# Optimization experiments

Measured on AMD Instinct MI355X. Metric: run time of the kernel, lower is better.

The kernel has to match this reference:

```python
import jax, jax.numpy as jnp
import numpy as np

CURV = 0.9            # geoopt PoincareBall(0.9)
SQRT_C = CURV ** 0.5
MIN_NORM = 1e-15
PROJ_EPS = 4e-3       # geoopt float32 boundary eps
ATANH_EPS = 1e-7
COS_EPS = 1e-8        # torch.cosine_similarity eps


def _norm(x):
    return jnp.sqrt(jnp.maximum(jnp.sum(x * x, axis=-1, keepdims=True), MIN_NORM * MIN_NORM))


def _project(x):
    # project onto ball of radius (1-eps)/sqrt(c)
    n = jnp.maximum(_norm(x), MIN_NORM)
    maxnorm = (1.0 - PROJ_EPS) / SQRT_C
    return jnp.where(n > maxnorm, x / n * maxnorm, x)


def expmap0(u):
    n = jnp.maximum(_norm(u), MIN_NORM)
    gamma = jnp.tanh(SQRT_C * n) * u / (SQRT_C * n)
    return _project(gamma)


def mobius_add(x, y):
    c = CURV
    x2 = jnp.sum(x * x, axis=-1, keepdims=True)
    y2 = jnp.sum(y * y, axis=-1, keepdims=True)
    xy = jnp.sum(x * y, axis=-1, keepdims=True)
    num = (1.0 + 2.0 * c * xy + c * y2) * x + (1.0 - c * x2) * y
    den = 1.0 + 2.0 * c * xy + c * c * x2 * y2
    return num / jnp.maximum(den, MIN_NORM)


def pdist(x, y):
    # dist(x,y) = 2/sqrt(c) * artanh(sqrt(c) * ||(-x) (+) y||)
    d = mobius_add(-x, y)
    n = _norm(d)[..., 0]
    z = jnp.clip(SQRT_C * n, -1.0 + ATANH_EPS, 1.0 - ATANH_EPS)
    return 2.0 / SQRT_C * jnp.arctanh(z)


def cos_sim(a, b):
    na = jnp.maximum(jnp.sqrt(jnp.sum(a * a, axis=-1)), COS_EPS)
    nb = jnp.maximum(jnp.sqrt(jnp.sum(b * b, axis=-1)), COS_EPS)
    return jnp.sum(a * b, axis=-1) / (na * nb)


def setup_inputs() -> dict:
    key = jax.random.key(0)
    ks = jax.random.split(key, 11)
    B, L, Ls, C, Lc, H, R = 4, 512, 128, 20, 128, 768, 512
    s = 0.02  # keep projected embeddings in a realistic range
    return {
        "text_out": jax.random.normal(ks[0], (B, L, H), jnp.float32),
        "summary_out": jax.random.normal(ks[1], (B, Ls, H), jnp.float32),
        "candidate_out": jax.random.normal(ks[2], (B, C, Lc, H), jnp.float32),
        "W_d": jax.random.normal(ks[3], (H, R), jnp.float32) * s,
        "W_s": jax.random.normal(ks[4], (H, R), jnp.float32) * s,
        "W_c": jax.random.normal(ks[5], (H, R), jnp.float32) * s,
        "W_p": jax.random.normal(ks[6], (R, R), jnp.float32) * s,
        "conv_w1": jax.random.normal(ks[7], (1, H, R), jnp.float32) * s,
        "conv_b1": jax.random.normal(ks[8], (R,), jnp.float32) * s,
        "conv_w2": jax.random.normal(ks[9], (2, H, R), jnp.float32) * s,
        "conv_b2": jax.random.normal(ks[10], (R,), jnp.float32) * s,
    }


def _forward(text_out, summary_out, candidate_out, W_d, W_s, W_c, W_p,
             conv_w1, conv_b1, conv_w2, conv_b2):
    # --- document ---
    doc_emb = expmap0(text_out[:, 0, :] @ W_d)                       # [B,R]

    # NGramers (max_gram=2, eval mode so dropout is identity)
    x = text_out[:, 1:-1, :]                                         # [B,L-2,H]
    y1 = jax.nn.relu(jnp.einsum('blh,hr->blr', x, conv_w1[0]) + conv_b1)
    y2 = jax.nn.relu(jnp.einsum('blh,hr->blr', x[:, :-1], conv_w2[0])
                     + jnp.einsum('blh,hr->blr', x[:, 1:], conv_w2[1]) + conv_b2)
    gram = jnp.concatenate([y1, y2], axis=1)                         # [B,2L-5,R]

    doc_word_emb = expmap0(jnp.einsum('blr,rk->blk', gram, W_p))     # [B,T,R]
    doc_inter = 1.0 / pdist(doc_word_emb, doc_emb[:, None, :])       # [B,T]

    # --- summary ---
    summary_emb = expmap0(jnp.max(summary_out, axis=1) @ W_s)        # [B,R]
    summary_score = -pdist(summary_emb, doc_emb) ** 2                # [B]
    sum_inter = 1.0 / pdist(doc_word_emb, summary_emb[:, None, :])   # [B,T]
    summary_score = summary_score + cos_sim(doc_inter, sum_inter)    # [B]

    # --- candidates ---
    cand_emb = expmap0(jnp.einsum('bch,hr->bcr', jnp.max(candidate_out, axis=2), W_c))  # [B,C,R]
    score = -pdist(cand_emb, doc_emb[:, None, :]) ** 2               # [B,C]
    cand_inter = 1.0 / pdist(doc_word_emb[:, None, :, :], cand_emb[:, :, None, :])      # [B,C,T]
    score = score + cos_sim(doc_inter[:, None, :], cand_inter)       # [B,C]
    return score, summary_score


def reference(text_out, summary_out, candidate_out, W_d, W_s, W_c, W_p,
              conv_w1, conv_b1, conv_w2, conv_b2):
    return _forward(text_out, summary_out, candidate_out, W_d, W_s, W_c, W_p,
                    conv_w1, conv_b1, conv_w2, conv_b2)
```

## Files before the change

kernel.cpp:

```cpp
#include <hip/hip_runtime.h>
#include <math.h>

#define SQRTC  0.94868329805051381f
#define MAXN   (0.996f/SQRTC)
#define OME_CLIP (1.0f - 0.996f*0.996f)
#define TWO_OVER_SQRTC 2.1081851067789197f

typedef unsigned short u16;
typedef __attribute__((ext_vector_type(8))) short bf8;
typedef __attribute__((ext_vector_type(4))) float f4;

__device__ __forceinline__ u16 f2bf(float f){
    union { float f; unsigned int i; } v; v.f = f;
    unsigned int x = v.i;
    unsigned int lsb = (x >> 16) & 1u;
    x += 0x7fffu + lsb;
    return (u16)(x >> 16);
}
__device__ __forceinline__ float bf2f(u16 u){
    union { unsigned int i; float f; } v; v.i = ((unsigned int)u) << 16; return v.f;
}

__device__ __forceinline__ void gload16(void* lds, const void* g){
    __builtin_amdgcn_global_load_lds(
        (const __attribute__((address_space(1))) unsigned int*)g,
        (__attribute__((address_space(3))) unsigned int*)lds,
        16, 0, 0);
}

__device__ __forceinline__ float pdist_stable(float ome_x, float ome_y, float t){
    float u = 1.0f - ome_x, v = 1.0f - ome_y;
    float den = fmaxf(1.0f - 1.8f*t + u*v, 1e-15f);
    float q = ome_x*ome_y/den;
    q = fminf(fmaxf(q, 2.0e-7f), 1.0f);
    float z = sqrtf(fmaxf(1.0f - q, 0.0f));
    float at = 0.5f * logf((1.0f+z)*(1.0f+z)/q);
    return TWO_OVER_SQRTC * at;
}

__device__ __forceinline__ void expmap_scale_ome(float sum, float* fout, float* omeout){
    float nraw = sqrtf(fmaxf(sum, 1e-30f));
    float n = fmaxf(nraw, 1e-15f);
    float sn = SQRTC*n;
    float th = tanhf(sn);
    float factor = th/sn;
    float gn = factor*nraw;
    if (gn > MAXN){ *fout = factor*(MAXN/gn); *omeout = OME_CLIP; }
    else { *fout = factor; *omeout = fmaxf((1.0f-th)*(1.0f+th), 1e-12f); }
}

__global__ __launch_bounds__(256)
void k_stage1(const float* __restrict__ summ, const float* __restrict__ cand,
              const float* __restrict__ text,
              const float* __restrict__ w1, const float* __restrict__ w2,
              const float* __restrict__ wp,
              float* __restrict__ smax, float* __restrict__ cmax,
              u16* __restrict__ textb, u16* __restrict__ w1t,
              u16* __restrict__ w2t, u16* __restrict__ wpt)
{
    __shared__ float shm[1056];
    int bx = blockIdx.x;
    int t = threadIdx.x;
    if (bx < 252){
        int row = bx / 3, hc = bx - row*3;
        int w = t >> 6, lane = t & 63;
        const float* in = (row < 4) ? (summ + (long long)row*128*768)
                                    : (cand + (long long)(row-4)*128*768);
        const float* p = in + (long long)(w*32)*768 + hc*256 + lane*4;
        float4 m = make_float4(-INFINITY,-INFINITY,-INFINITY,-INFINITY);
        #pragma unroll 8
        for (int l = 0; l < 32; l++){
            float4 v = *(const float4*)(p + (long long)l*768);
            m.x = fmaxf(m.x, v.x); m.y = fmaxf(m.y, v.y);
            m.z = fmaxf(m.z, v.z); m.w = fmaxf(m.w, v.w);
        }
        float4* sm4 = (float4*)shm;
        sm4[w*64 + lane] = m; __syncthreads();
        if (t < 64){
            float4 a = sm4[t], b4 = sm4[64+t], c4 = sm4[128+t], d4 = sm4[192+t];
            float4 r;
            r.x = fmaxf(fmaxf(a.x,b4.x), fmaxf(c4.x,d4.x));
            r.y = fmaxf(fmaxf(a.y,b4.y), fmaxf(c4.y,d4.y));
            r.z = fmaxf(fmaxf(a.z,b4.z), fmaxf(c4.z,d4.z));
            r.w = fmaxf(fmaxf(a.w,b4.w), fmaxf(c4.w,d4.w));
            float* outp = (row < 4) ? (smax + row*768) : (cmax + (row-4)*768);
            *(float4*)(outp + hc*256 + t*4) = r;
        }
        return;
    }
    int pb = bx - 252;
    if (pb < 768){
        int base = pb*2048 + t*8;
        float4 a = *(const float4*)(text + base);
        float4 b = *(const float4*)(text + base + 4);
        *(ushort4*)(textb + base)     = make_ushort4(f2bf(a.x), f2bf(a.y), f2bf(a.z), f2bf(a.w));
        *(ushort4*)(textb + base + 4) = make_ushort4(f2bf(b.x), f2bf(b.y), f2bf(b.z), f2bf(b.w));
        return;
    }
    int j = pb - 768;
    const float* in; u16* outp; int K;
    if (j < 384){ in = w1; outp = w1t; K = 768; }
    else if (j < 1152){ j -= 384; in = w2; outp = w2t; K = 1536; }
    else { j -= 1152; in = wp; outp = wpt; K = 512; }
    const int N = 512, ntile = N/32;
    int k0 = (j/ntile)*32, n0 = (j - (j/ntile)*ntile)*32;
    int tx = t & 31, ty = t >> 5;
    #pragma unroll
    for (int i = 0; i < 4; i++)
        shm[(ty*4+i)*33 + tx] = in[(long long)(k0 + ty*4 + i)*N + n0 + tx];
    __syncthreads();
    #pragma unroll
    for (int i = 0; i < 4; i++)
        outp[(long long)(n0 + ty*4 + i)*K + k0 + tx] = f2bf(shm[tx*33 + ty*4+i]);
}

__global__ __launch_bounds__(256)
void k_stage2(const u16* __restrict__ textb,
              const u16* __restrict__ w1t, const u16* __restrict__ w2t,
              const float* __restrict__ cb1, const float* __restrict__ cb2,
              const float* __restrict__ text,
              const float* __restrict__ smax, const float* __restrict__ cmax,
              const float* __restrict__ W_d, const float* __restrict__ W_s,
              const float* __restrict__ W_c,
              u16* __restrict__ gram, float* __restrict__ emb_all)
{
    __shared__ char smem[32768];
    int bx = blockIdx.x;
    int t = threadIdx.x;
    if (bx < 512){
        u16* As0 = (u16*)smem;
        u16* Bs0 = (u16*)(smem + 8192);
        u16* As1 = (u16*)(smem + 16384);
        u16* Bs1 = (u16*)(smem + 24576);
        int xx = bx & 63, yy = bx >> 6;
        int job = xx & 1;
        int m0 = (xx >> 1) * 64;
        int n0 = yy * 64;
        int K   = job ? 1536 : 768;
        int M   = job ? 2036 : 2040;
        int rpb = job ? 509 : 510;
        int ob  = job ? 510 : 0;
        const u16* Bt = job ? w2t : w1t;
        const float* bias = job ? cb2 : cb1;

        int r0 = t >> 3;
        int co = (((t & 7) ^ (r0 & 7)) << 3);

        int gm0 = m0 + r0;      if (gm0 >= M) gm0 = M - 1;
        int gm1 = m0 + r0 + 32; if (gm1 >= M) gm1 = M - 1;
        int ab0 = gm0 / rpb, al0 = gm0 - ab0*rpb;
        int ab1 = gm1 / rpb, al1 = gm1 - ab1*rpb;
        const u16* a0 = textb + (long long)ab0*393216 + (long long)(al0+1)*768 + co;
        const u16* a1 = textb + (long long)ab1*393216 + (long long)(al1+1)*768 + co;
        const u16* bp0 = Bt + (long long)(n0 + r0)*K      + co;
        const u16* bp1 = Bt + (long long)(n0 + r0 + 32)*K + co;
        int d0 = t*8, d1 = (256 + t)*8;

        int lane = t & 63, wv = t >> 6;
        int fm = lane & 15, fq = lane >> 4;
        int arow = wv*16 + fm;
        int aswz = arow & 7, bswz = fm & 7;
        int aoff0 = arow*64 + ((fq     ^ aswz) << 3);
        int aoff1 = arow*64 + (((4+fq) ^ aswz) << 3);
        int boff0 = ((fq     ^ bswz) << 3);
        int boff1 = (((4+fq) ^ bswz) << 3);

        f4 acc0 = {0,0,0,0}, acc1 = {0,0,0,0}, acc2 = {0,0,0,0}, acc3 = {0,0,0,0};
        const int nt = K >> 6;
        gload16(As0 + d0, a0);
        gload16(As0 + d1, a1);
        gload16(Bs0 + d0, bp0);
        gload16(Bs0 + d1, bp1);
        for (int i = 0; i < nt; i++){
            u16* Ac = (i & 1) ? As1 : As0;
            u16* Bc = (i & 1) ? Bs1 : Bs0;
            if (i + 1 < nt){
                u16* An = (i & 1) ? As0 : As1;
                u16* Bn = (i & 1) ? Bs0 : Bs1;
                int kn = (i + 1) << 6;
                gload16(An + d0, a0 + kn);
                gload16(An + d1, a1 + kn);
                gload16(Bn + d0, bp0 + kn);
                gload16(Bn + d1, bp1 + kn);
                asm volatile("s_waitcnt vmcnt(4)" ::: "memory");
            } else {
                asm volatile("s_waitcnt vmcnt(0)" ::: "memory");
            }
            __builtin_amdgcn_s_barrier();
            bf8 af0 = *(const bf8*)(Ac + aoff0);
            bf8 af1 = *(const bf8*)(Ac + aoff1);
            bf8 b00 = *(const bf8*)(Bc + (fm   )*64 + boff0);
            bf8 b10 = *(const bf8*)(Bc + (16+fm)*64 + boff0);
            bf8 b20 = *(const bf8*)(Bc + (32+fm)*64 + boff0);
            bf8 b30 = *(const bf8*)(Bc + (48+fm)*64 + boff0);
            bf8 b01 = *(const bf8*)(Bc + (fm   )*64 + boff1);
            bf8 b11 = *(const bf8*)(Bc + (16+fm)*64 + boff1);
            bf8 b21 = *(const bf8*)(Bc + (32+fm)*64 + boff1);
            bf8 b31 = *(const bf8*)(Bc + (48+fm)*64 + boff1);
            acc0 = __builtin_amdgcn_mfma_f32_16x16x32_bf16(af0, b00, acc0, 0, 0, 0);
            acc1 = __builtin_amdgcn_mfma_f32_16x16x32_bf16(af0, b10, acc1, 0, 0, 0);
            acc2 = __builtin_amdgcn_mfma_f32_16x16x32_bf16(af0, b20, acc2, 0, 0, 0);
            acc3 = __builtin_amdgcn_mfma_f32_16x16x32_bf16(af0, b30, acc3, 0, 0, 0);
            acc0 = __builtin_amdgcn_mfma_f32_16x16x32_bf16(af1, b01, acc0, 0, 0, 0);
            acc1 = __builtin_amdgcn_mfma_f32_16x16x32_bf16(af1, b11, acc1, 0, 0, 0);
            acc2 = __builtin_amdgcn_mfma_f32_16x16x32_bf16(af1, b21, acc2, 0, 0, 0);
            acc3 = __builtin_amdgcn_mfma_f32_16x16x32_bf16(af1, b31, acc3, 0, 0, 0);
            __builtin_amdgcn_s_barrier();
        }
        int col = n0 + fm;
        float bv0 = bias[col], bv1 = bias[col+16], bv2 = bias[col+32], bv3 = bias[col+48];
        #pragma unroll
        for (int i = 0; i < 4; i++){
            int row = m0 + wv*16 + fq*4 + i;
            if (row >= M) continue;
            int b = row/rpb, l = row - b*rpb;
            long long orow = (long long)b*1019 + ob + l;
            u16* gp = gram + orow*512;
            gp[col]      = f2bf(fmaxf(acc0[i] + bv0, 0.f));
            gp[col + 16] = f2bf(fmaxf(acc1[i] + bv1, 0.f));
            gp[col + 32] = f2bf(fmaxf(acc2[i] + bv2, 0.f));
            gp[col + 48] = f2bf(fmaxf(acc3[i] + bv3, 0.f));
        }
        return;
    }
    {
        int eb = bx - 512;
        int row = eb >> 3, nt = eb & 7;
        float* a   = (float*)smem;
        float* red = (float*)smem + 768;
        const float* A; const float* W;
        if (row < 4){ A = text + (long long)row*512*768; W = W_d; }
        else if (row < 8){ A = smax + (long long)(row-4)*768; W = W_s; }
        else { A = cmax + (long long)(row-8)*768; W = W_c; }
        for (int k = t; k < 768; k += 256) a[k] = A[k];
        __syncthreads();
        int lane = t & 63, kg = t >> 6;
        int col = nt*64 + lane;
        const float* Wp = W + (long long)(kg*192)*512 + col;
        float acc = 0.f;
        #pragma unroll 8
        for (int k = 0; k < 192; k++) acc += a[kg*192 + k] * Wp[k*512];
        red[t] = acc; __syncthreads();
        if (t < 64) emb_all[(long long)row*512 + col] = red[t] + red[t+64] + red[t+128] + red[t+192];
    }
}

__global__ __launch_bounds__(256)
void k_stage3(const u16* __restrict__ gram, const u16* __restrict__ wpt,
              u16* __restrict__ dwe_b,
              float* __restrict__ emb_all, float* __restrict__ ome_all,
              u16* __restrict__ emb_b)
{
    __shared__ char smem[32768];
    int bx = blockIdx.x;
    int t = threadIdx.x;
    if (bx < 512){
        u16* As0 = (u16*)smem;
        u16* Bs0 = (u16*)(smem + 8192);
        u16* As1 = (u16*)(smem + 16384);
        u16* Bs1 = (u16*)(smem + 24576);
        const int K = 512, M = 4076;
        int m0 = (bx >> 3) * 64;
        int n0 = (bx & 7) * 64;

        int r0 = t >> 3;
        int co = (((t & 7) ^ (r0 & 7)) << 3);
        int gm0 = m0 + r0;      if (gm0 >= M) gm0 = M - 1;
        int gm1 = m0 + r0 + 32; if (gm1 >= M) gm1 = M - 1;
        const u16* a0 = gram + (long long)gm0*512 + co;
        const u16* a1 = gram + (long long)gm1*512 + co;
        const u16* bp0 = wpt + (long long)(n0 + r0)*K      + co;
        const u16* bp1 = wpt + (long long)(n0 + r0 + 32)*K + co;
        int d0 = t*8, d1 = (256 + t)*8;

        int lane = t & 63, wv = t >> 6;
        int fm = lane & 15, fq = lane >> 4;
        int arow = wv*16 + fm;
        int aswz = arow & 7, bswz = fm & 7;
        int aoff0 = arow*64 + ((fq     ^ aswz) << 3);
        int aoff1 = arow*64 + (((4+fq) ^ aswz) << 3);
        int boff0 = ((fq     ^ bswz) << 3);
        int boff1 = (((4+fq) ^ bswz) << 3);

        f4 acc0 = {0,0,0,0}, acc1 = {0,0,0,0}, acc2 = {0,0,0,0}, acc3 = {0,0,0,0};
        const int nt = K >> 6;
        gload16(As0 + d0, a0);
        gload16(As0 + d1, a1);
        gload16(Bs0 + d0, bp0);
        gload16(Bs0 + d1, bp1);
        for (int i = 0; i < nt; i++){
            u16* Ac = (i & 1) ? As1 : As0;
            u16* Bc = (i & 1) ? Bs1 : Bs0;
            if (i + 1 < nt){
                u16* An = (i & 1) ? As0 : As1;
                u16* Bn = (i & 1) ? Bs0 : Bs1;
                int kn = (i + 1) << 6;
                gload16(An + d0, a0 + kn);
                gload16(An + d1, a1 + kn);
                gload16(Bn + d0, bp0 + kn);
                gload16(Bn + d1, bp1 + kn);
                asm volatile("s_waitcnt vmcnt(4)" ::: "memory");
            } else {
                asm volatile("s_waitcnt vmcnt(0)" ::: "memory");
            }
            __builtin_amdgcn_s_barrier();
            bf8 af0 = *(const bf8*)(Ac + aoff0);
            bf8 af1 = *(const bf8*)(Ac + aoff1);
            bf8 b00 = *(const bf8*)(Bc + (fm   )*64 + boff0);
            bf8 b10 = *(const bf8*)(Bc + (16+fm)*64 + boff0);
            bf8 b20 = *(const bf8*)(Bc + (32+fm)*64 + boff0);
            bf8 b30 = *(const bf8*)(Bc + (48+fm)*64 + boff0);
            bf8 b01 = *(const bf8*)(Bc + (fm   )*64 + boff1);
            bf8 b11 = *(const bf8*)(Bc + (16+fm)*64 + boff1);
            bf8 b21 = *(const bf8*)(Bc + (32+fm)*64 + boff1);
            bf8 b31 = *(const bf8*)(Bc + (48+fm)*64 + boff1);
            acc0 = __builtin_amdgcn_mfma_f32_16x16x32_bf16(af0, b00, acc0, 0, 0, 0);
            acc1 = __builtin_amdgcn_mfma_f32_16x16x32_bf16(af0, b10, acc1, 0, 0, 0);
            acc2 = __builtin_amdgcn_mfma_f32_16x16x32_bf16(af0, b20, acc2, 0, 0, 0);
            acc3 = __builtin_amdgcn_mfma_f32_16x16x32_bf16(af0, b30, acc3, 0, 0, 0);
            acc0 = __builtin_amdgcn_mfma_f32_16x16x32_bf16(af1, b01, acc0, 0, 0, 0);
            acc1 = __builtin_amdgcn_mfma_f32_16x16x32_bf16(af1, b11, acc1, 0, 0, 0);
            acc2 = __builtin_amdgcn_mfma_f32_16x16x32_bf16(af1, b21, acc2, 0, 0, 0);
            acc3 = __builtin_amdgcn_mfma_f32_16x16x32_bf16(af1, b31, acc3, 0, 0, 0);
            __builtin_amdgcn_s_barrier();
        }
        int col = n0 + fm;
        #pragma unroll
        for (int i = 0; i < 4; i++){
            int row = m0 + wv*16 + fq*4 + i;
            if (row >= M) continue;
            u16* dp = dwe_b + (long long)row*512;
            dp[col]      = f2bf(acc0[i]);
            dp[col + 16] = f2bf(acc1[i]);
            dp[col + 32] = f2bf(acc2[i]);
            dp[col + 48] = f2bf(acc3[i]);
        }
        return;
    }
    {
        float* red = (float*)smem;
        int row = bx - 512;
        float* X = emb_all + (long long)row*512;
        float2 u = *(float2*)(X + t*2);
        red[t] = u.x*u.x + u.y*u.y; __syncthreads();
        for (int s = 128; s > 0; s >>= 1){ if (t < s) red[t] += red[t+s]; __syncthreads(); }
        float f, ome;
        expmap_scale_ome(red[0], &f, &ome);
        float sx = u.x*f, sy = u.y*f;
        *(float2*)(X + t*2) = make_float2(sx, sy);
        u16* Xb = emb_b + (long long)row*512;
        Xb[t*2]   = f2bf(sx);
        Xb[t*2+1] = f2bf(sy);
        if (t == 0) ome_all[row] = ome;
    }
}

__global__ __launch_bounds__(64)
void k_dots_mfma(const u16* __restrict__ dwe_b, const u16* __restrict__ emb_b,
                 const float* __restrict__ ome_all,
                 float* __restrict__ doc_inter, float* __restrict__ sum_inter,
                 float* __restrict__ cand_inter)
{
    int bx = blockIdx.x;
    int b  = bx >> 6;
    int m0 = (bx & 63) * 16;
    int t = threadIdx.x;
    int fm = t & 15, fq = t >> 4;

    int arow = m0 + fm; if (arow > 1018) arow = 1018;
    const u16* Ap = dwe_b + ((long long)(b*1019 + arow))*512 + fq*8;

    int n1 = 16 + fm; if (n1 > 21) n1 = 21;
    int e0 = (fm == 0) ? b : (fm == 1) ? 4 + b : 8 + b*20 + (fm - 2);
    int e1 = 8 + b*20 + (n1 - 2);
    const u16* B0 = emb_b + (long long)e0*512 + fq*8;
    const u16* B1 = emb_b + (long long)e1*512 + fq*8;
    float oy0 = ome_all[e0];
    float oy1 = ome_all[e1];

    f4 acc0 = {0,0,0,0}, acc1 = {0,0,0,0};
    float ssq = 0.f;
    #pragma unroll 4
    for (int k0 = 0; k0 < 512; k0 += 32){
        bf8 av  = *(const bf8*)(Ap + k0);
        bf8 bv0 = *(const bf8*)(B0 + k0);
        bf8 bv1 = *(const bf8*)(B1 + k0);
        #pragma unroll
        for (int j = 0; j < 8; j++){ float x = bf2f(((u16*)&av)[j]); ssq += x*x; }
        acc0 = __builtin_amdgcn_mfma_f32_16x16x32_bf16(av, bv0, acc0, 0, 0, 0);
        acc1 = __builtin_amdgcn_mfma_f32_16x16x32_bf16(av, bv1, acc1, 0, 0, 0);
    }
    ssq += __shfl_xor(ssq, 16);
    ssq += __shfl_xor(ssq, 32);

    #pragma unroll
    for (int i = 0; i < 4; i++){
        int r = fq*4 + i;
        float rs = __shfl(ssq, r);
        int row = m0 + r;
        if (row >= 1019) continue;
        float f, ox;
        expmap_scale_ome(rs, &f, &ox);
        long long grow = (long long)b*1019 + row;
        {
            float s = acc0[i] * f;
            float dist = pdist_stable(ox, oy0, s);
            float inv = 1.0f/fmaxf(dist, 1e-12f);
            if (fm == 0) doc_inter[grow] = inv;
            else if (fm == 1) sum_inter[grow] = inv;
            else cand_inter[((long long)(b*20 + (fm - 2)))*1019 + row] = inv;
        }
        if (16 + fm < 22){
            float s = acc1[i] * f;
            float dist = pdist_stable(ox, oy1, s);
            float inv = 1.0f/fmaxf(dist, 1e-12f);
            cand_inter[((long long)(b*20 + (16 + fm - 2)))*1019 + row] = inv;
        }
    }
}

__global__ __launch_bounds__(256)
void k_final(const float* __restrict__ doc_inter, const float* __restrict__ sum_inter,
             const float* __restrict__ cand_inter,
             const float* __restrict__ emb_all, const float* __restrict__ ome_all,
             float* __restrict__ out)
{
    __shared__ float r0[256], r1[256], r2[256], r3[256];
    int j = blockIdx.x, t = threadIdx.x;
    int b; const float *a, *bb; int xi, yi; int outIdx;
    if (j < 80){
        b = j/20;
        a  = doc_inter + b*1019;
        bb = cand_inter + (long long)j*1019;
        xi = 8 + j; yi = b;
        outIdx = j;
    } else {
        b = j - 80;
        a  = doc_inter + b*1019;
        bb = sum_inter + b*1019;
        xi = 4 + b; yi = b;
        outIdx = 80 + b;
    }
    const float* xe = emb_all + (long long)xi*512;
    const float* ye = emb_all + (long long)yi*512;
    float ox = ome_all[xi], oy = ome_all[yi];
    float saa = 0.f, sbb = 0.f, sab = 0.f, st = 0.f;
    for (int l = t; l < 1019; l += 256){ float av = a[l], bv = bb[l]; saa += av*av; sbb += bv*bv; sab += av*bv; }
    for (int k = t; k < 512; k += 256) st += xe[k]*ye[k];
    r0[t] = saa; r1[t] = sbb; r2[t] = sab; r3[t] = st; __syncthreads();
    for (int s = 128; s > 0; s >>= 1){
        if (t < s){ r0[t] += r0[t+s]; r1[t] += r1[t+s]; r2[t] += r2[t+s]; r3[t] += r3[t+s]; }
        __syncthreads();
    }
    if (t == 0){
        float na = fmaxf(sqrtf(r0[0]), 1e-8f);
        float nb = fmaxf(sqrtf(r1[0]), 1e-8f);
        float cosv = r2[0] / (na*nb);
        float pd = pdist_stable(ox, oy, r3[0]);
        out[outIdx] = -pd*pd + cosv;
    }
}

extern "C" void kernel_launch(void* const* d_in, const int* in_sizes, int n_in,
                              void* d_out, int out_size, void* d_ws, size_t ws_size,
                              hipStream_t stream) {
    const float* text = (const float*)d_in[0];
    const float* summ = (const float*)d_in[1];
    const float* cand = (const float*)d_in[2];
    const float* W_d  = (const float*)d_in[3];
    const float* W_s  = (const float*)d_in[4];
    const float* W_c  = (const float*)d_in[5];
    const float* W_p  = (const float*)d_in[6];
    const float* cw1  = (const float*)d_in[7];
    const float* cb1  = (const float*)d_in[8];
    const float* cw2  = (const float*)d_in[9];
    const float* cb2  = (const float*)d_in[10];
    float* out = (float*)d_out;

    const int B = 4, C = 20, H = 768;

    char* base = (char*)d_ws;
    size_t off = 0;
    auto allocF = [&](size_t n)->float*{ float* p = (float*)(base + off); off += ((n*4) + 255) & ~(size_t)255; return p; };
    auto allocU = [&](size_t n)->u16*{ u16* p = (u16*)(base + off); off += ((n*2) + 255) & ~(size_t)255; return p; };

    float* smax = allocF(B*H);
    float* cmax = allocF(B*C*H);
    float* emb_all = allocF(88*512);
    float* ome_all = allocF(88);
    u16* emb_b = allocU(88*512);
    u16* textb = allocU(4*512*768);
    u16* w1t   = allocU(512*768);
    u16* w2t   = allocU(512*1536);
    u16* wpt   = allocU(512*512);
    u16* gram  = allocU(4076*512);
    u16* dwe_b = allocU(4076*512);
    float* doc_inter = allocF(4076);
    float* sum_inter = allocF(4076);
    float* cand_inter= allocF(B*C*1019);

    k_stage1<<<2428, 256, 0, stream>>>(summ, cand, text, cw1, cw2, W_p,
                                       smax, cmax, textb, w1t, w2t, wpt);

    k_stage2<<<1216, 256, 0, stream>>>(textb, w1t, w2t, cb1, cb2,
                                       text, smax, cmax, W_d, W_s, W_c,
                                       gram, emb_all);

    k_stage3<<<600, 256, 0, stream>>>(gram, wpt, dwe_b, emb_all, ome_all, emb_b);

    k_dots_mfma<<<256, 64, 0, stream>>>(dwe_b, emb_b, ome_all,
                                        doc_inter, sum_inter, cand_inter);

    k_final<<<84, 256, 0, stream>>>(doc_inter, sum_inter, cand_inter,
                                    emb_all, ome_all, out);
}
```

Baseline: 139.9 us.

## Fuse final cosine/pdist reduction into MFMA dots kernel via atomics and last-block finish

Removes the k_final launch and the doc/sum/cand_inter intermediate buffers. Each dots block now reduces its per-row inverse distances into squared-norm and dot-product partial sums and adds them to a small global accumulator with atomics. A ticket counter lets the last block compute the cosine similarities and final scores, and block 0 also computes the embedding dot products. This saves one kernel launch and the global round trip, at the cost of atomic contention, a serial 84-iteration loop in block 0, and float atomics whose order is not deterministic.

```diff
diff --git a/kernel.cpp b/kernel.cpp
--- a/kernel.cpp
+++ b/kernel.cpp
@@ -49,6 +49,14 @@
     else { *fout = factor; *omeout = fmaxf((1.0f-th)*(1.0f+th), 1e-12f); }
 }
 
+#define ACC_SDD 0
+#define ACC_SSS 4
+#define ACC_SDS 8
+#define ACC_SCC 12
+#define ACC_SDC 92
+#define ACC_CTR 172
+#define ACC_PD  176
+
 __global__ __launch_bounds__(256)
 void k_stage1(const float* __restrict__ summ, const float* __restrict__ cand,
               const float* __restrict__ text,
@@ -56,11 +64,13 @@
               const float* __restrict__ wp,
               float* __restrict__ smax, float* __restrict__ cmax,
               u16* __restrict__ textb, u16* __restrict__ w1t,
-              u16* __restrict__ w2t, u16* __restrict__ wpt)
+              u16* __restrict__ w2t, u16* __restrict__ wpt,
+              float* __restrict__ accum)
 {
     __shared__ float shm[1056];
     int bx = blockIdx.x;
     int t = threadIdx.x;
+    if (bx == 0 && t < 176) accum[t] = 0.0f;
     if (bx < 252){
         int row = bx / 3, hc = bx - row*3;
         int w = t >> 6, lane = t & 63;
@@ -357,9 +367,8 @@
 
 __global__ __launch_bounds__(64)
 void k_dots_mfma(const u16* __restrict__ dwe_b, const u16* __restrict__ emb_b,
-                 const float* __restrict__ ome_all,
-                 float* __restrict__ doc_inter, float* __restrict__ sum_inter,
-                 float* __restrict__ cand_inter)
+                 const float* __restrict__ ome_all, const float* __restrict__ emb_all,
+                 float* __restrict__ accum, float* __restrict__ out)
 {
     int bx = blockIdx.x;
     int b  = bx >> 6;
@@ -393,71 +402,89 @@
     ssq += __shfl_xor(ssq, 16);
     ssq += __shfl_xor(ssq, 32);
 
+    float cc0 = 0.f, dc0 = 0.f, cc1 = 0.f, dc1 = 0.f;
     #pragma unroll
     for (int i = 0; i < 4; i++){
         int r = fq*4 + i;
         float rs = __shfl(ssq, r);
         int row = m0 + r;
-        if (row >= 1019) continue;
         float f, ox;
         expmap_scale_ome(rs, &f, &ox);
-        long long grow = (long long)b*1019 + row;
+        float inv0, inv1;
         {
             float s = acc0[i] * f;
             float dist = pdist_stable(ox, oy0, s);
-            float inv = 1.0f/fmaxf(dist, 1e-12f);
-            if (fm == 0) doc_inter[grow] = inv;
-            else if (fm == 1) sum_inter[grow] = inv;
-            else cand_inter[((long long)(b*20 + (fm - 2)))*1019 + row] = inv;
-        }
-        if (16 + fm < 22){
+            inv0 = 1.0f/fmaxf(dist, 1e-12f);
+        }
+        {
             float s = acc1[i] * f;
             float dist = pdist_stable(ox, oy1, s);
-            float inv = 1.0f/fmaxf(dist, 1e-12f);
-            cand_inter[((long long)(b*20 + (16 + fm - 2)))*1019 + row] = inv;
-        }
-    }
-}
-
-__global__ __launch_bounds__(256)
-void k_final(const float* __restrict__ doc_inter, const float* __restrict__ sum_inter,
-             const float* __restrict__ cand_inter,
-             const float* __restrict__ emb_all, const float* __restrict__ ome_all,
-             float* __restrict__ out)
-{
-    __shared__ float r0[256], r1[256], r2[256], r3[256];
-    int j = blockIdx.x, t = threadIdx.x;
-    int b; const float *a, *bb; int xi, yi; int outIdx;
-    if (j < 80){
-        b = j/20;
-        a  = doc_inter + b*1019;
-        bb = cand_inter + (long long)j*1019;
-        xi = 8 + j; yi = b;
-        outIdx = j;
-    } else {
-        b = j - 80;
-        a  = doc_inter + b*1019;
-        bb = sum_inter + b*1019;
-        xi = 4 + b; yi = b;
-        outIdx = 80 + b;
-    }
-    const float* xe = emb_all + (long long)xi*512;
-    const float* ye = emb_all + (long long)yi*512;
-    float ox = ome_all[xi], oy = ome_all[yi];
-    float saa = 0.f, sbb = 0.f, sab = 0.f, st = 0.f;
-    for (int l = t; l < 1019; l += 256){ float av = a[l], bv = bb[l]; saa += av*av; sbb += bv*bv; sab += av*bv; }
-    for (int k = t; k < 512; k += 256) st += xe[k]*ye[k];
-    r0[t] = saa; r1[t] = sbb; r2[t] = sab; r3[t] = st; __syncthreads();
-    for (int s = 128; s > 0; s >>= 1){
-        if (t < s){ r0[t] += r0[t+s]; r1[t] += r1[t+s]; r2[t] += r2[t+s]; r3[t] += r3[t+s]; }
-        __syncthreads();
-    }
-    if (t == 0){
-        float na = fmaxf(sqrtf(r0[0]), 1e-8f);
-        float nb = fmaxf(sqrtf(r1[0]), 1e-8f);
-        float cosv = r2[0] / (na*nb);
-        float pd = pdist_stable(ox, oy, r3[0]);
-        out[outIdx] = -pd*pd + cosv;
+            inv1 = 1.0f/fmaxf(dist, 1e-12f);
+        }
+        float dv = __shfl(inv0, t & 48);
+        if (row < 1019){
+            cc0 += inv0*inv0; dc0 += inv0*dv;
+            cc1 += inv1*inv1; dc1 += inv1*dv;
+        }
+    }
+    cc0 += __shfl_xor(cc0, 16); cc0 += __shfl_xor(cc0, 32);
+    dc0 += __shfl_xor(dc0, 16); dc0 += __shfl_xor(dc0, 32);
+    cc1 += __shfl_xor(cc1, 16); cc1 += __shfl_xor(cc1, 32);
+    dc1 += __shfl_xor(dc1, 16); dc1 += __shfl_xor(dc1, 32);
+    if (t < 16){
+        if (fm == 0)      atomicAdd(&accum[ACC_SDD + b], cc0);
+        else if (fm == 1){ atomicAdd(&accum[ACC_SSS + b], cc0);
+                           atomicAdd(&accum[ACC_SDS + b], dc0); }
+        else { atomicAdd(&accum[ACC_SCC + b*20 + fm - 2], cc0);
+               atomicAdd(&accum[ACC_SDC + b*20 + fm - 2], dc0); }
+        if (fm < 6){ atomicAdd(&accum[ACC_SCC + b*20 + 14 + fm], cc1);
+                     atomicAdd(&accum[ACC_SDC + b*20 + 14 + fm], dc1); }
+    }
+
+    if (bx == 0){
+        for (int j = 0; j < 84; j++){
+            int xi = (j < 80) ? 8 + j : 4 + (j - 80);
+            int yi = (j < 80) ? j/20  : (j - 80);
+            const float* xe = emb_all + (long long)xi*512 + t*8;
+            const float* ye = emb_all + (long long)yi*512 + t*8;
+            float s = 0.f;
+            #pragma unroll
+            for (int q = 0; q < 8; q++) s += xe[q]*ye[q];
+            s += __shfl_xor(s, 1);  s += __shfl_xor(s, 2);
+            s += __shfl_xor(s, 4);  s += __shfl_xor(s, 8);
+            s += __shfl_xor(s, 16); s += __shfl_xor(s, 32);
+            if (t == 0) accum[ACC_PD + j] = s;
+        }
+    }
+
+    __threadfence();
+    int old = 0;
+    if (t == 0) old = (int)atomicAdd((unsigned int*)&accum[ACC_CTR], 1u);
+    old = __shfl(old, 0);
+    if (old == 255){
+        __threadfence();
+        for (int j = t; j < 84; j += 64){
+            int b_, xi, yi; float saa, sbb, sab;
+            if (j < 80){
+                b_ = j/20;
+                saa = atomicAdd(&accum[ACC_SDD + b_], 0.f);
+                sbb = atomicAdd(&accum[ACC_SCC + j], 0.f);
+                sab = atomicAdd(&accum[ACC_SDC + j], 0.f);
+                xi = 8 + j; yi = b_;
+            } else {
+                b_ = j - 80;
+                saa = atomicAdd(&accum[ACC_SDD + b_], 0.f);
+                sbb = atomicAdd(&accum[ACC_SSS + b_], 0.f);
+                sab = atomicAdd(&accum[ACC_SDS + b_], 0.f);
+                xi = 4 + b_; yi = b_;
+            }
+            float pdot = atomicAdd(&accum[ACC_PD + j], 0.f);
+            float na = fmaxf(sqrtf(saa), 1e-8f);
+            float nb = fmaxf(sqrtf(sbb), 1e-8f);
+            float cosv = sab / (na*nb);
+            float pd = pdist_stable(ome_all[xi], ome_all[yi], pdot);
+            out[j] = -pd*pd + cosv;
+        }
     }
 }
 
@@ -488,6 +515,7 @@
     float* cmax = allocF(B*C*H);
     float* emb_all = allocF(88*512);
     float* ome_all = allocF(88);
+    float* accum   = allocF(272);
     u16* emb_b = allocU(88*512);
     u16* textb = allocU(4*512*768);
     u16* w1t   = allocU(512*768);
@@ -495,12 +523,9 @@
     u16* wpt   = allocU(512*512);
     u16* gram  = allocU(4076*512);
     u16* dwe_b = allocU(4076*512);
-    float* doc_inter = allocF(4076);
-    float* sum_inter = allocF(4076);
-    float* cand_inter= allocF(B*C*1019);
 
     k_stage1<<<2428, 256, 0, stream>>>(summ, cand, text, cw1, cw2, W_p,
-                                       smax, cmax, textb, w1t, w2t, wpt);
+                                       smax, cmax, textb, w1t, w2t, wpt, accum);
 
     k_stage2<<<1216, 256, 0, stream>>>(textb, w1t, w2t, cb1, cb2,
                                        text, smax, cmax, W_d, W_s, W_c,
@@ -508,9 +533,6 @@
 
     k_stage3<<<600, 256, 0, stream>>>(gram, wpt, dwe_b, emb_all, ome_all, emb_b);
 
-    k_dots_mfma<<<256, 64, 0, stream>>>(dwe_b, emb_b, ome_all,
-                                        doc_inter, sum_inter, cand_inter);
-
-    k_final<<<84, 256, 0, stream>>>(doc_inter, sum_inter, cand_inter,
-                                    emb_all, ome_all, out);
-}
+    k_dots_mfma<<<256, 64, 0, stream>>>(dwe_b, emb_b, ome_all, emb_all,
+                                        accum, out);
+}
```

Result: slower. 182.7 us (+30.6%).
